# Kernel optimization log

Measured on AMD Instinct MI355X. Metric: run time of the kernel, lower is better.

## Reference

```python
import jax, jax.numpy as jnp
import numpy as np
import math

B, S, HID = 2, 2048, 512
HEADS = 8
DH = HID // HEADS  # 64


def _euler_alpha(seq_len, dh):
    # alpha[t, i] = t * 10000^(-2i/dh), shape [S, dh//2]
    pos = jnp.arange(seq_len, dtype=jnp.float32)[:, None]
    ids = jnp.arange(dh // 2, dtype=jnp.float32)
    freq = jnp.power(10000.0, -2.0 * ids / dh)
    return pos * freq  # [S, dh//2]


def euler_rotate(x, delta):
    # x: [B, H, S, DH] -> polar rotation (EulerFormer, type='ro', no bias b)
    r = x[..., ::2]
    p = x[..., 1::2]
    lam = jnp.sqrt(r * r + p * p)
    theta = jnp.arctan2(p, r) * delta + _euler_alpha(x.shape[2], x.shape[3])[None, None]
    r2 = lam * jnp.cos(theta)
    p2 = lam * jnp.sin(theta)
    # interleave back: stack last dim then reshape
    out = jnp.stack([r2, p2], axis=-1)
    return out.reshape(x.shape)


def setup_inputs() -> dict:
    key = jax.random.key(0)
    ks = jax.random.split(key, 12)
    sc = 1.0 / math.sqrt(HID)
    return {
        "q": jax.random.normal(ks[0], (B, S, HID), jnp.float32),
        "k": jax.random.normal(ks[1], (B, S, HID), jnp.float32),
        "v": jax.random.normal(ks[2], (B, S, HID), jnp.float32),
        "Wq": jax.random.normal(ks[3], (HID, HID), jnp.float32) * sc,
        "bq": jnp.zeros((HID,), jnp.float32),
        "Wk": jax.random.normal(ks[4], (HID, HID), jnp.float32) * sc,
        "bk": jnp.zeros((HID,), jnp.float32),
        "Wv": jax.random.normal(ks[5], (HID, HID), jnp.float32) * sc,
        "bv": jnp.zeros((HID,), jnp.float32),
        "Wo": jax.random.normal(ks[6], (HID, HID), jnp.float32) * sc,
        "bo": jnp.zeros((HID,), jnp.float32),
        "delta_q": jnp.ones((1,), jnp.float32),
        "delta_k": jnp.ones((1,), jnp.float32),
    }


def reference(q, k, v, Wq, bq, Wk, bk, Wv, bv, Wo, bo, delta_q, delta_k):
    b = q.shape[0]
    def proj(x, W, bias):
        y = x @ W.T + bias  # torch Linear: x W^T + b
        return y.reshape(b, -1, HEADS, DH).transpose(0, 2, 1, 3)  # [B,H,S,DH]
    qh = proj(q, Wq, bq)
    kh = proj(k, Wk, bk)
    vh = proj(v, Wv, bv)
    qh = euler_rotate(qh, delta_q)
    kh = euler_rotate(kh, delta_k)
    corr = jnp.einsum('bhqd,bhkd->bhqk', qh, kh) / math.sqrt(DH)
    s = corr.shape[-1]
    causal = jnp.triu(jnp.full((s, s), -jnp.inf, jnp.float32), k=1)
    corr = corr + causal[None, None]
    attn = jax.nn.softmax(corr, axis=-1)
    hidden = jnp.einsum('bhqk,bhkd->bhqd', attn, vh)
    hidden = hidden.transpose(0, 2, 1, 3).reshape(b, -1, HID)
    return hidden @ Wo.T + bo
```

## Files before the change

kernel.cpp:

```cpp
#include <hip/hip_runtime.h>
#include <math.h>

constexpr int B_   = 2;
constexpr int S_   = 2048;
constexpr int HID_ = 512;
constexpr int H_   = 8;
constexpr int DH_  = 64;
constexpr int M_   = B_ * S_;

typedef unsigned short ushort_t;
typedef unsigned int   uint_t;
typedef __attribute__((ext_vector_type(4))) float  f32x4;
typedef __attribute__((ext_vector_type(8))) __bf16 bf16x8;
typedef __attribute__((ext_vector_type(4))) uint_t u32x4;

#define MFMA16(A, Bv, C) __builtin_amdgcn_mfma_f32_16x16x32_bf16( \
    __builtin_bit_cast(bf16x8, (A)), __builtin_bit_cast(bf16x8, (Bv)), (C), 0, 0, 0)

__device__ __forceinline__ uint2 splitPair(float x0, float x1) {
    uint_t b0 = __float_as_uint(x0), b1 = __float_as_uint(x1);
    uint_t hi = (b0 >> 16) | (b1 & 0xFFFF0000u);
    float h0 = __uint_as_float(b0 & 0xFFFF0000u);
    float h1 = __uint_as_float(b1 & 0xFFFF0000u);
    uint_t l0 = __float_as_uint(x0 - h0), l1 = __float_as_uint(x1 - h1);
    uint_t lo = (l0 >> 16) | (l1 & 0xFFFF0000u);
    return make_uint2(hi, lo);
}

template <int MODE>
__device__ __forceinline__ void gemm_mfma_body(const float* __restrict__ A,
                                               const float* __restrict__ W,
                                               const float* __restrict__ bias,
                                               float* __restrict__ out)
{
    constexpr int K_ = HID_;
    __shared__ __align__(16) ushort_t Ah[64][40],  Al[64][40];
    __shared__ __align__(16) ushort_t Bh[128][40], Bl[128][40];

    const int t    = threadIdx.x;
    const int lane = t & 63;
    const int wid  = t >> 6;
    const int wr   = wid >> 1;
    const int wc   = wid & 1;
    const int a    = lane & 15;
    const int g    = lane >> 4;
    const int bm   = blockIdx.x * 64;
    const int bn   = blockIdx.y * 128;

    f32x4 acc[2][4];
#pragma unroll
    for (int mt = 0; mt < 2; ++mt)
#pragma unroll
        for (int nt = 0; nt < 4; ++nt)
#pragma unroll
            for (int r = 0; r < 4; ++r) acc[mt][nt][r] = 0.f;

    const int arow = t >> 2, ag8 = t & 3;

    for (int k0 = 0; k0 < K_; k0 += 32) {
        __syncthreads();
        {
            const float* p = A + (size_t)(bm + arow) * K_ + k0 + ag8 * 8;
            const float4 x0 = *(const float4*)p;
            const float4 x1 = *(const float4*)(p + 4);
            const uint2 s0 = splitPair(x0.x, x0.y), s1 = splitPair(x0.z, x0.w);
            const uint2 s2 = splitPair(x1.x, x1.y), s3 = splitPair(x1.z, x1.w);
            *(u32x4*)&Ah[arow][ag8 * 8] = u32x4{s0.x, s1.x, s2.x, s3.x};
            *(u32x4*)&Al[arow][ag8 * 8] = u32x4{s0.y, s1.y, s2.y, s3.y};
        }
#pragma unroll
        for (int i = 0; i < 2; ++i) {
            const int seg = t + i * 256;
            const int row = seg >> 2, g8 = seg & 3;
            const float* p = W + (size_t)(bn + row) * K_ + k0 + g8 * 8;
            const float4 x0 = *(const float4*)p;
            const float4 x1 = *(const float4*)(p + 4);
            const uint2 s0 = splitPair(x0.x, x0.y), s1 = splitPair(x0.z, x0.w);
            const uint2 s2 = splitPair(x1.x, x1.y), s3 = splitPair(x1.z, x1.w);
            *(u32x4*)&Bh[row][g8 * 8] = u32x4{s0.x, s1.x, s2.x, s3.x};
            *(u32x4*)&Bl[row][g8 * 8] = u32x4{s0.y, s1.y, s2.y, s3.y};
        }
        __syncthreads();

        u32x4 afh[2], afl[2];
#pragma unroll
        for (int mt = 0; mt < 2; ++mt) {
            const int ar = wr * 32 + mt * 16 + a;
            afh[mt] = *(const u32x4*)&Ah[ar][g * 8];
            afl[mt] = *(const u32x4*)&Al[ar][g * 8];
        }
#pragma unroll
        for (int nt = 0; nt < 4; ++nt) {
            const int br = wc * 64 + nt * 16 + a;
            const u32x4 bfh = *(const u32x4*)&Bh[br][g * 8];
            const u32x4 bfl = *(const u32x4*)&Bl[br][g * 8];
#pragma unroll
            for (int mt = 0; mt < 2; ++mt) {
                acc[mt][nt] = MFMA16(afh[mt], bfh, acc[mt][nt]);
                acc[mt][nt] = MFMA16(afh[mt], bfl, acc[mt][nt]);
                acc[mt][nt] = MFMA16(afl[mt], bfh, acc[mt][nt]);
            }
        }
    }

#pragma unroll
    for (int mt = 0; mt < 2; ++mt) {
#pragma unroll
        for (int nt = 0; nt < 4; ++nt) {
            const int n = bn + wc * 64 + nt * 16 + a;
            const float bb = bias[n];
#pragma unroll
            for (int r = 0; r < 4; ++r) {
                const int m = bm + wr * 32 + mt * 16 + g * 4 + r;
                const float val = acc[mt][nt][r] + bb;
                if (MODE == 0) {
                    out[(size_t)m * HID_ + n] = val;
                } else {
                    const int b = m >> 11;
                    const int s = m & (S_ - 1);
                    const int h = n >> 6;
                    const int d = n & (DH_ - 1);
                    if (MODE == 1)
                        out[(((size_t)b * H_ + h) * S_ + s) * DH_ + d] = val;
                    else
                        out[(((size_t)b * H_ + h) * DH_ + d) * S_ + s] = val;
                }
            }
        }
    }
}

struct QkvPtrs {
    const float* A[3];
    const float* W[3];
    const float* bias[3];
    float*       out[3];
};

__global__ __launch_bounds__(256)
void gemm_qkv_kernel(QkvPtrs p)
{
    const int z = blockIdx.z;
    if (z == 2) gemm_mfma_body<2>(p.A[2], p.W[2], p.bias[2], p.out[2]);
    else        gemm_mfma_body<1>(p.A[z], p.W[z], p.bias[z], p.out[z]);
}

__global__ __launch_bounds__(256)
void gemm_out_kernel(const float* __restrict__ A, const float* __restrict__ W,
                     const float* __restrict__ bias, float* __restrict__ out)
{
    gemm_mfma_body<0>(A, W, bias, out);
}

__global__ __launch_bounds__(256)
void euler_rot_kernel(float* __restrict__ qh, float* __restrict__ kh,
                      const float* __restrict__ dq, const float* __restrict__ dk)
{
    constexpr int NP = B_ * H_ * S_ * (DH_ / 2);
    const int idx = blockIdx.x * 256 + threadIdx.x;

    float* x; float delta; int pi;
    if (idx < NP) { x = qh; delta = dq[0]; pi = idx; }
    else          { x = kh; delta = dk[0]; pi = idx - NP; }

    const int i = pi & 31;
    const int s = (pi >> 5) & (S_ - 1);
    const float freq = exp2f(-(float)i * 0.4152410118609203f);

    const float2 rp = ((const float2*)x)[pi];
    const float lam = sqrtf(rp.x * rp.x + rp.y * rp.y);
    const float th  = atan2f(rp.y, rp.x) * delta + (float)s * freq;
    float sn, cs;
    sincosf(th, &sn, &cs);
    ((float2*)x)[pi] = make_float2(lam * cs, lam * sn);
}

__global__ __launch_bounds__(256)
void attn_mfma_kernel(const float* __restrict__ qh, const float* __restrict__ kh,
                      const float* __restrict__ vt, float* __restrict__ hidden)
{
    __shared__ __align__(16) ushort_t Khi[64][72];
    __shared__ __align__(16) ushort_t Klo[64][72];
    __shared__ __align__(16) ushort_t Vhi[64][72];
    __shared__ __align__(16) ushort_t Vlo[64][72];
    __shared__ __align__(16) ushort_t Ph[4][16][72];
    __shared__ __align__(16) ushort_t Pl[4][16][72];

    const int t    = threadIdx.x;
    const int lane = t & 63;
    const int wid  = t >> 6;
    const int a    = lane & 15;
    const int g    = lane >> 4;
    const int qt   = 31 - blockIdx.x;
    const int bh   = blockIdx.y;

    const float* Qrow = qh + ((size_t)bh * S_ + (size_t)qt * 64 + wid * 16 + a) * DH_;
    u32x4 qhi[2], qlo[2];
#pragma unroll
    for (int kit = 0; kit < 2; ++kit) {
        const float* p = Qrow + kit * 32 + g * 8;
        const float4 x0 = *(const float4*)p;
        const float4 x1 = *(const float4*)(p + 4);
        const uint2 p0 = splitPair(x0.x * 0.125f, x0.y * 0.125f);
        const uint2 p1 = splitPair(x0.z * 0.125f, x0.w * 0.125f);
        const uint2 p2 = splitPair(x1.x * 0.125f, x1.y * 0.125f);
        const uint2 p3 = splitPair(x1.z * 0.125f, x1.w * 0.125f);
        qhi[kit] = u32x4{p0.x, p1.x, p2.x, p3.x};
        qlo[kit] = u32x4{p0.y, p1.y, p2.y, p3.y};
    }

    f32x4 Oacc[4];
#pragma unroll
    for (int nt = 0; nt < 4; ++nt)
#pragma unroll
        for (int r = 0; r < 4; ++r) Oacc[nt][r] = 0.f;
    float mrow[4] = {-INFINITY, -INFINITY, -INFINITY, -INFINITY};
    float lrow[4] = {0.f, 0.f, 0.f, 0.f};

    const float4* Kg = (const float4*)(kh + (size_t)bh * S_ * DH_);
    const float*  Vg = vt + (size_t)bh * DH_ * S_;

    for (int kt = 0; kt <= qt; ++kt) {
        __syncthreads();
#pragma unroll
        for (int i = 0; i < 4; ++i) {
            const int flat = t + i * 256;
            const int key = flat >> 4, d4 = (flat & 15) * 4;
            const float4 kv = Kg[kt * 1024 + flat];
            const uint2 s01 = splitPair(kv.x, kv.y);
            const uint2 s23 = splitPair(kv.z, kv.w);
            *(uint2*)&Khi[key][d4] = make_uint2(s01.x, s23.x);
            *(uint2*)&Klo[key][d4] = make_uint2(s01.y, s23.y);
        }
#pragma unroll
        for (int i = 0; i < 4; ++i) {
            const int flat = t + i * 256;
            const int dh = flat >> 4, k4 = (flat & 15) * 4;
            const float4 vv = *(const float4*)(Vg + (size_t)dh * S_ + kt * 64 + k4);
            const uint2 s01 = splitPair(vv.x, vv.y);
            const uint2 s23 = splitPair(vv.z, vv.w);
            *(uint2*)&Vhi[dh][k4] = make_uint2(s01.x, s23.x);
            *(uint2*)&Vlo[dh][k4] = make_uint2(s01.y, s23.y);
        }
        __syncthreads();

        f32x4 Sacc[4];
#pragma unroll
        for (int nt = 0; nt < 4; ++nt)
#pragma unroll
            for (int r = 0; r < 4; ++r) Sacc[nt][r] = 0.f;
#pragma unroll
        for (int kit = 0; kit < 2; ++kit) {
#pragma unroll
            for (int nt = 0; nt < 4; ++nt) {
                const u32x4 kbh = *(const u32x4*)&Khi[a + 16 * nt][kit * 32 + g * 8];
                const u32x4 kbl = *(const u32x4*)&Klo[a + 16 * nt][kit * 32 + g * 8];
                Sacc[nt] = MFMA16(qhi[kit], kbh, Sacc[nt]);
                Sacc[nt] = MFMA16(qhi[kit], kbl, Sacc[nt]);
                Sacc[nt] = MFMA16(qlo[kit], kbh, Sacc[nt]);
            }
        }

        float sc[4][4];
        const int q0 = qt * 64 + wid * 16 + g * 4;
        const int k0 = kt * 64 + a;
#pragma unroll
        for (int nt = 0; nt < 4; ++nt)
#pragma unroll
            for (int r = 0; r < 4; ++r)
                sc[nt][r] = (k0 + 16 * nt <= q0 + r) ? Sacc[nt][r] : -INFINITY;

#pragma unroll
        for (int r = 0; r < 4; ++r) {
            float mr = fmaxf(fmaxf(sc[0][r], sc[1][r]), fmaxf(sc[2][r], sc[3][r]));
            mr = fmaxf(mr, __shfl_xor(mr, 1));
            mr = fmaxf(mr, __shfl_xor(mr, 2));
            mr = fmaxf(mr, __shfl_xor(mr, 4));
            mr = fmaxf(mr, __shfl_xor(mr, 8));
            const float mnew = fmaxf(mrow[r], mr);
            const float fac  = __expf(mrow[r] - mnew);
            mrow[r] = mnew;
            float ps = 0.f;
            const int q = g * 4 + r;
#pragma unroll
            for (int nt = 0; nt < 4; ++nt) {
                const float p = __expf(sc[nt][r] - mnew);
                ps += p;
                const uint_t pb = __float_as_uint(p);
                Ph[wid][q][a + 16 * nt] = (ushort_t)(pb >> 16);
                const float phf = __uint_as_float(pb & 0xFFFF0000u);
                Pl[wid][q][a + 16 * nt] = (ushort_t)(__float_as_uint(p - phf) >> 16);
            }
            lrow[r] = lrow[r] * fac + ps;
#pragma unroll
            for (int nt = 0; nt < 4; ++nt) Oacc[nt][r] *= fac;
        }

#pragma unroll
        for (int kit = 0; kit < 2; ++kit) {
            const u32x4 pah = *(const u32x4*)&Ph[wid][a][kit * 32 + g * 8];
            const u32x4 pal = *(const u32x4*)&Pl[wid][a][kit * 32 + g * 8];
#pragma unroll
            for (int nt = 0; nt < 4; ++nt) {
                const u32x4 vbh = *(const u32x4*)&Vhi[a + 16 * nt][kit * 32 + g * 8];
                const u32x4 vbl = *(const u32x4*)&Vlo[a + 16 * nt][kit * 32 + g * 8];
                Oacc[nt] = MFMA16(pah, vbh, Oacc[nt]);
                Oacc[nt] = MFMA16(pah, vbl, Oacc[nt]);
                Oacc[nt] = MFMA16(pal, vbh, Oacc[nt]);
            }
        }
    }

    float inv[4];
#pragma unroll
    for (int r = 0; r < 4; ++r) {
        float ls = lrow[r];
        ls += __shfl_xor(ls, 1);
        ls += __shfl_xor(ls, 2);
        ls += __shfl_xor(ls, 4);
        ls += __shfl_xor(ls, 8);
        inv[r] = 1.f / ls;
    }
    const int b = bh >> 3, h = bh & 7;
#pragma unroll
    for (int r = 0; r < 4; ++r) {
        const int qg = qt * 64 + wid * 16 + g * 4 + r;
        float* dst = hidden + ((size_t)b * S_ + qg) * HID_ + h * DH_ + a;
#pragma unroll
        for (int nt = 0; nt < 4; ++nt) dst[16 * nt] = Oacc[nt][r] * inv[r];
    }
}

extern "C" void kernel_launch(void* const* d_in, const int* in_sizes, int n_in,
                              void* d_out, int out_size, void* d_ws, size_t ws_size,
                              hipStream_t stream)
{
    const float* q  = (const float*)d_in[0];
    const float* k  = (const float*)d_in[1];
    const float* v  = (const float*)d_in[2];
    const float* Wq = (const float*)d_in[3];
    const float* bq = (const float*)d_in[4];
    const float* Wk = (const float*)d_in[5];
    const float* bk = (const float*)d_in[6];
    const float* Wv = (const float*)d_in[7];
    const float* bv = (const float*)d_in[8];
    const float* Wo = (const float*)d_in[9];
    const float* bo = (const float*)d_in[10];
    const float* dq = (const float*)d_in[11];
    const float* dk = (const float*)d_in[12];
    float* out = (float*)d_out;

    float* ws = (float*)d_ws;
    const size_t TEN = (size_t)B_ * S_ * HID_;
    float* qh     = ws;
    float* kh     = ws + TEN;
    float* vtr    = ws + 2 * TEN;
    float* hidden = ws + 3 * TEN;

    QkvPtrs p;
    p.A[0] = q; p.W[0] = Wq; p.bias[0] = bq; p.out[0] = qh;
    p.A[1] = k; p.W[1] = Wk; p.bias[1] = bk; p.out[1] = kh;
    p.A[2] = v; p.W[2] = Wv; p.bias[2] = bv; p.out[2] = vtr;

    gemm_qkv_kernel<<<dim3(M_ / 64, HID_ / 128, 3), 256, 0, stream>>>(p);
    euler_rot_kernel<<<(2 * B_ * H_ * S_ * (DH_ / 2)) / 256, 256, 0, stream>>>(qh, kh, dq, dk);
    attn_mfma_kernel<<<dim3(S_ / 64, B_ * H_), 256, 0, stream>>>(qh, kh, vtr, hidden);
    gemm_out_kernel<<<dim3(M_ / 64, HID_ / 128), 256, 0, stream>>>(hidden, Wo, bo, out);
}
```

Before: 268.7 us.

## Fuse Euler rotation and bf16 hi/lo split into QKV GEMM epilogue

Moves the Euler polar rotation and the Q scaling into the QKV projection epilogue, pairing values across lanes with a shuffle. The GEMM now writes pre-split bf16 hi/lo tensors, so the separate rotation kernel goes away and attention loads ready-made fragments instead of converting fp32 on every tile. The GEMM tile shrinks from 64x128 to 64x64 to launch more blocks, and the next K-slice is prefetched into registers while the current one is stored to shared memory. Risks: scattered 2-byte stores in the epilogue, and the trig work now runs inside the GEMM blocks.

```diff
diff --git a/kernel.cpp b/kernel.cpp
--- a/kernel.cpp
+++ b/kernel.cpp
@@ -27,15 +27,25 @@
     return make_uint2(hi, lo);
 }
 
+__device__ __forceinline__ void splitOne(float x, ushort_t& hi, ushort_t& lo) {
+    uint_t b = __float_as_uint(x);
+    hi = (ushort_t)(b >> 16);
+    float h = __uint_as_float(b & 0xFFFF0000u);
+    lo = (ushort_t)(__float_as_uint(x - h) >> 16);
+}
+
 template <int MODE>
 __device__ __forceinline__ void gemm_mfma_body(const float* __restrict__ A,
                                                const float* __restrict__ W,
                                                const float* __restrict__ bias,
-                                               float* __restrict__ out)
+                                               ushort_t* __restrict__ outHi,
+                                               ushort_t* __restrict__ outLo,
+                                               float* __restrict__ outF,
+                                               const float* __restrict__ delta)
 {
     constexpr int K_ = HID_;
-    __shared__ __align__(16) ushort_t Ah[64][40],  Al[64][40];
-    __shared__ __align__(16) ushort_t Bh[128][40], Bl[128][40];
+    __shared__ __align__(16) ushort_t Ah[64][40], Al[64][40];
+    __shared__ __align__(16) ushort_t Bh[64][40], Bl[64][40];
 
     const int t    = threadIdx.x;
     const int lane = t & 63;
@@ -45,44 +55,44 @@
     const int a    = lane & 15;
     const int g    = lane >> 4;
     const int bm   = blockIdx.x * 64;
-    const int bn   = blockIdx.y * 128;
-
-    f32x4 acc[2][4];
+    const int bn   = blockIdx.y * 64;
+
+    const int srow = t >> 2, sg8 = t & 3;
+    const float* Ap = A + (size_t)(bm + srow) * K_ + sg8 * 8;
+    const float* Wp = W + (size_t)(bn + srow) * K_ + sg8 * 8;
+
+    float4 ra0 = *(const float4*)Ap,       ra1 = *(const float4*)(Ap + 4);
+    float4 rb0 = *(const float4*)Wp,       rb1 = *(const float4*)(Wp + 4);
+
+    f32x4 acc[2][2];
 #pragma unroll
     for (int mt = 0; mt < 2; ++mt)
 #pragma unroll
-        for (int nt = 0; nt < 4; ++nt)
+        for (int nt = 0; nt < 2; ++nt)
 #pragma unroll
             for (int r = 0; r < 4; ++r) acc[mt][nt][r] = 0.f;
-
-    const int arow = t >> 2, ag8 = t & 3;
 
     for (int k0 = 0; k0 < K_; k0 += 32) {
         __syncthreads();
         {
-            const float* p = A + (size_t)(bm + arow) * K_ + k0 + ag8 * 8;
-            const float4 x0 = *(const float4*)p;
-            const float4 x1 = *(const float4*)(p + 4);
-            const uint2 s0 = splitPair(x0.x, x0.y), s1 = splitPair(x0.z, x0.w);
-            const uint2 s2 = splitPair(x1.x, x1.y), s3 = splitPair(x1.z, x1.w);
-            *(u32x4*)&Ah[arow][ag8 * 8] = u32x4{s0.x, s1.x, s2.x, s3.x};
-            *(u32x4*)&Al[arow][ag8 * 8] = u32x4{s0.y, s1.y, s2.y, s3.y};
-        }
-#pragma unroll
-        for (int i = 0; i < 2; ++i) {
-            const int seg = t + i * 256;
-            const int row = seg >> 2, g8 = seg & 3;
-            const float* p = W + (size_t)(bn + row) * K_ + k0 + g8 * 8;
-            const float4 x0 = *(const float4*)p;
-            const float4 x1 = *(const float4*)(p + 4);
-            const uint2 s0 = splitPair(x0.x, x0.y), s1 = splitPair(x0.z, x0.w);
-            const uint2 s2 = splitPair(x1.x, x1.y), s3 = splitPair(x1.z, x1.w);
-            *(u32x4*)&Bh[row][g8 * 8] = u32x4{s0.x, s1.x, s2.x, s3.x};
-            *(u32x4*)&Bl[row][g8 * 8] = u32x4{s0.y, s1.y, s2.y, s3.y};
+            const uint2 s0 = splitPair(ra0.x, ra0.y), s1 = splitPair(ra0.z, ra0.w);
+            const uint2 s2 = splitPair(ra1.x, ra1.y), s3 = splitPair(ra1.z, ra1.w);
+            *(u32x4*)&Ah[srow][sg8 * 8] = u32x4{s0.x, s1.x, s2.x, s3.x};
+            *(u32x4*)&Al[srow][sg8 * 8] = u32x4{s0.y, s1.y, s2.y, s3.y};
+            const uint2 t0 = splitPair(rb0.x, rb0.y), t1 = splitPair(rb0.z, rb0.w);
+            const uint2 t2 = splitPair(rb1.x, rb1.y), t3 = splitPair(rb1.z, rb1.w);
+            *(u32x4*)&Bh[srow][sg8 * 8] = u32x4{t0.x, t1.x, t2.x, t3.x};
+            *(u32x4*)&Bl[srow][sg8 * 8] = u32x4{t0.y, t1.y, t2.y, t3.y};
+        }
+        if (k0 + 32 < K_) {
+            const float* pa = Ap + k0 + 32;
+            const float* pw = Wp + k0 + 32;
+            ra0 = *(const float4*)pa; ra1 = *(const float4*)(pa + 4);
+            rb0 = *(const float4*)pw; rb1 = *(const float4*)(pw + 4);
         }
         __syncthreads();
 
-        u32x4 afh[2], afl[2];
+        u32x4 afh[2], afl[2], bfh[2], bfl[2];
 #pragma unroll
         for (int mt = 0; mt < 2; ++mt) {
             const int ar = wr * 32 + mt * 16 + a;
@@ -90,41 +100,72 @@
             afl[mt] = *(const u32x4*)&Al[ar][g * 8];
         }
 #pragma unroll
-        for (int nt = 0; nt < 4; ++nt) {
-            const int br = wc * 64 + nt * 16 + a;
-            const u32x4 bfh = *(const u32x4*)&Bh[br][g * 8];
-            const u32x4 bfl = *(const u32x4*)&Bl[br][g * 8];
+        for (int nt = 0; nt < 2; ++nt) {
+            const int br = wc * 32 + nt * 16 + a;
+            bfh[nt] = *(const u32x4*)&Bh[br][g * 8];
+            bfl[nt] = *(const u32x4*)&Bl[br][g * 8];
+        }
+#pragma unroll
+        for (int nt = 0; nt < 2; ++nt)
 #pragma unroll
             for (int mt = 0; mt < 2; ++mt) {
-                acc[mt][nt] = MFMA16(afh[mt], bfh, acc[mt][nt]);
-                acc[mt][nt] = MFMA16(afh[mt], bfl, acc[mt][nt]);
-                acc[mt][nt] = MFMA16(afl[mt], bfh, acc[mt][nt]);
-            }
-        }
-    }
-
+                acc[mt][nt] = MFMA16(afh[mt], bfh[nt], acc[mt][nt]);
+                acc[mt][nt] = MFMA16(afh[mt], bfl[nt], acc[mt][nt]);
+                acc[mt][nt] = MFMA16(afl[mt], bfh[nt], acc[mt][nt]);
+            }
+    }
+
+    const float del = (MODE == 1 || MODE == 2) ? delta[0] : 0.f;
 #pragma unroll
     for (int mt = 0; mt < 2; ++mt) {
 #pragma unroll
-        for (int nt = 0; nt < 4; ++nt) {
-            const int n = bn + wc * 64 + nt * 16 + a;
+        for (int nt = 0; nt < 2; ++nt) {
+            const int n  = bn + wc * 32 + nt * 16 + a;
             const float bb = bias[n];
-#pragma unroll
-            for (int r = 0; r < 4; ++r) {
-                const int m = bm + wr * 32 + mt * 16 + g * 4 + r;
-                const float val = acc[mt][nt][r] + bb;
-                if (MODE == 0) {
-                    out[(size_t)m * HID_ + n] = val;
-                } else {
-                    const int b = m >> 11;
-                    const int s = m & (S_ - 1);
-                    const int h = n >> 6;
-                    const int d = n & (DH_ - 1);
-                    if (MODE == 1)
-                        out[(((size_t)b * H_ + h) * S_ + s) * DH_ + d] = val;
-                    else
-                        out[(((size_t)b * H_ + h) * DH_ + d) * S_ + s] = val;
+            f32x4 vals;
+#pragma unroll
+            for (int r = 0; r < 4; ++r) vals[r] = acc[mt][nt][r] + bb;
+
+            if (MODE == 0) {
+#pragma unroll
+                for (int r = 0; r < 4; ++r) {
+                    const int m = bm + wr * 32 + mt * 16 + g * 4 + r;
+                    outF[(size_t)m * HID_ + n] = vals[r];
                 }
+            } else if (MODE == 1 || MODE == 2) {
+                const int d  = n & 63;
+                const int h  = n >> 6;
+                const float freq = exp2f(-(float)(d >> 1) * 0.4152410118609203f);
+#pragma unroll
+                for (int r = 0; r < 4; ++r) {
+                    const int m = bm + wr * 32 + mt * 16 + g * 4 + r;
+                    const int b = m >> 11, s = m & (S_ - 1);
+                    const float val  = vals[r];
+                    const float part = __shfl_xor(val, 1);
+                    const float rr = (a & 1) ? part : val;
+                    const float pp = (a & 1) ? val  : part;
+                    const float lam = sqrtf(rr * rr + pp * pp);
+                    const float th  = atan2f(pp, rr) * del + (float)s * freq;
+                    float sn, cs;
+                    sincosf(th, &sn, &cs);
+                    float o = (a & 1) ? lam * sn : lam * cs;
+                    if (MODE == 1) o *= 0.125f;
+                    ushort_t hi, lo;
+                    splitOne(o, hi, lo);
+                    const size_t idx = (((size_t)b * H_ + h) * S_ + s) * DH_ + d;
+                    outHi[idx] = hi;
+                    outLo[idx] = lo;
+                }
+            } else {
+                const int d  = n & 63;
+                const int h  = n >> 6;
+                const int m0 = bm + wr * 32 + mt * 16 + g * 4;
+                const int b  = m0 >> 11, s0 = m0 & (S_ - 1);
+                const uint2 p01 = splitPair(vals[0], vals[1]);
+                const uint2 p23 = splitPair(vals[2], vals[3]);
+                const size_t idx = (((size_t)b * H_ + h) * DH_ + d) * S_ + s0;
+                *(uint2*)&outHi[idx] = make_uint2(p01.x, p23.x);
+                *(uint2*)&outLo[idx] = make_uint2(p01.y, p23.y);
             }
         }
     }
@@ -134,50 +175,32 @@
     const float* A[3];
     const float* W[3];
     const float* bias[3];
-    float*       out[3];
+    ushort_t*    hi[3];
+    ushort_t*    lo[3];
+    const float* del[2];
 };
 
 __global__ __launch_bounds__(256)
 void gemm_qkv_kernel(QkvPtrs p)
 {
     const int z = blockIdx.z;
-    if (z == 2) gemm_mfma_body<2>(p.A[2], p.W[2], p.bias[2], p.out[2]);
-    else        gemm_mfma_body<1>(p.A[z], p.W[z], p.bias[z], p.out[z]);
+    if (z == 0)      gemm_mfma_body<1>(p.A[0], p.W[0], p.bias[0], p.hi[0], p.lo[0], nullptr, p.del[0]);
+    else if (z == 1) gemm_mfma_body<2>(p.A[1], p.W[1], p.bias[1], p.hi[1], p.lo[1], nullptr, p.del[1]);
+    else             gemm_mfma_body<3>(p.A[2], p.W[2], p.bias[2], p.hi[2], p.lo[2], nullptr, nullptr);
 }
 
 __global__ __launch_bounds__(256)
 void gemm_out_kernel(const float* __restrict__ A, const float* __restrict__ W,
                      const float* __restrict__ bias, float* __restrict__ out)
 {
-    gemm_mfma_body<0>(A, W, bias, out);
+    gemm_mfma_body<0>(A, W, bias, nullptr, nullptr, out, nullptr);
 }
 
 __global__ __launch_bounds__(256)
-void euler_rot_kernel(float* __restrict__ qh, float* __restrict__ kh,
-                      const float* __restrict__ dq, const float* __restrict__ dk)
-{
-    constexpr int NP = B_ * H_ * S_ * (DH_ / 2);
-    const int idx = blockIdx.x * 256 + threadIdx.x;
-
-    float* x; float delta; int pi;
-    if (idx < NP) { x = qh; delta = dq[0]; pi = idx; }
-    else          { x = kh; delta = dk[0]; pi = idx - NP; }
-
-    const int i = pi & 31;
-    const int s = (pi >> 5) & (S_ - 1);
-    const float freq = exp2f(-(float)i * 0.4152410118609203f);
-
-    const float2 rp = ((const float2*)x)[pi];
-    const float lam = sqrtf(rp.x * rp.x + rp.y * rp.y);
-    const float th  = atan2f(rp.y, rp.x) * delta + (float)s * freq;
-    float sn, cs;
-    sincosf(th, &sn, &cs);
-    ((float2*)x)[pi] = make_float2(lam * cs, lam * sn);
-}
-
-__global__ __launch_bounds__(256)
-void attn_mfma_kernel(const float* __restrict__ qh, const float* __restrict__ kh,
-                      const float* __restrict__ vt, float* __restrict__ hidden)
+void attn_mfma_kernel(const ushort_t* __restrict__ qhi_g, const ushort_t* __restrict__ qlo_g,
+                      const ushort_t* __restrict__ khi_g, const ushort_t* __restrict__ klo_g,
+                      const ushort_t* __restrict__ vhi_g, const ushort_t* __restrict__ vlo_g,
+                      float* __restrict__ hidden)
 {
     __shared__ __align__(16) ushort_t Khi[64][72];
     __shared__ __align__(16) ushort_t Klo[64][72];
@@ -194,19 +217,14 @@
     const int qt   = 31 - blockIdx.x;
     const int bh   = blockIdx.y;
 
-    const float* Qrow = qh + ((size_t)bh * S_ + (size_t)qt * 64 + wid * 16 + a) * DH_;
     u32x4 qhi[2], qlo[2];
-#pragma unroll
-    for (int kit = 0; kit < 2; ++kit) {
-        const float* p = Qrow + kit * 32 + g * 8;
-        const float4 x0 = *(const float4*)p;
-        const float4 x1 = *(const float4*)(p + 4);
-        const uint2 p0 = splitPair(x0.x * 0.125f, x0.y * 0.125f);
-        const uint2 p1 = splitPair(x0.z * 0.125f, x0.w * 0.125f);
-        const uint2 p2 = splitPair(x1.x * 0.125f, x1.y * 0.125f);
-        const uint2 p3 = splitPair(x1.z * 0.125f, x1.w * 0.125f);
-        qhi[kit] = u32x4{p0.x, p1.x, p2.x, p3.x};
-        qlo[kit] = u32x4{p0.y, p1.y, p2.y, p3.y};
+    {
+        const size_t qrow = ((size_t)bh * S_ + (size_t)qt * 64 + wid * 16 + a) * DH_;
+#pragma unroll
+        for (int kit = 0; kit < 2; ++kit) {
+            qhi[kit] = *(const u32x4*)&qhi_g[qrow + kit * 32 + g * 8];
+            qlo[kit] = *(const u32x4*)&qlo_g[qrow + kit * 32 + g * 8];
+        }
     }
 
     f32x4 Oacc[4];
@@ -217,30 +235,20 @@
     float mrow[4] = {-INFINITY, -INFINITY, -INFINITY, -INFINITY};
     float lrow[4] = {0.f, 0.f, 0.f, 0.f};
 
-    const float4* Kg = (const float4*)(kh + (size_t)bh * S_ * DH_);
-    const float*  Vg = vt + (size_t)bh * DH_ * S_;
-
     for (int kt = 0; kt <= qt; ++kt) {
+        const ushort_t* Ksh = khi_g + ((size_t)bh * S_ + kt * 64) * DH_;
+        const ushort_t* Ksl = klo_g + ((size_t)bh * S_ + kt * 64) * DH_;
+        const ushort_t* Vsh = vhi_g + (size_t)bh * DH_ * S_ + kt * 64;
+        const ushort_t* Vsl = vlo_g + (size_t)bh * DH_ * S_ + kt * 64;
         __syncthreads();
 #pragma unroll
-        for (int i = 0; i < 4; ++i) {
-            const int flat = t + i * 256;
-            const int key = flat >> 4, d4 = (flat & 15) * 4;
-            const float4 kv = Kg[kt * 1024 + flat];
-            const uint2 s01 = splitPair(kv.x, kv.y);
-            const uint2 s23 = splitPair(kv.z, kv.w);
-            *(uint2*)&Khi[key][d4] = make_uint2(s01.x, s23.x);
-            *(uint2*)&Klo[key][d4] = make_uint2(s01.y, s23.y);
-        }
-#pragma unroll
-        for (int i = 0; i < 4; ++i) {
-            const int flat = t + i * 256;
-            const int dh = flat >> 4, k4 = (flat & 15) * 4;
-            const float4 vv = *(const float4*)(Vg + (size_t)dh * S_ + kt * 64 + k4);
-            const uint2 s01 = splitPair(vv.x, vv.y);
-            const uint2 s23 = splitPair(vv.z, vv.w);
-            *(uint2*)&Vhi[dh][k4] = make_uint2(s01.x, s23.x);
-            *(uint2*)&Vlo[dh][k4] = make_uint2(s01.y, s23.y);
+        for (int i = 0; i < 2; ++i) {
+            const int seg = t + i * 256;
+            const int row = seg >> 3, c8 = (seg & 7) * 8;
+            *(u32x4*)&Khi[row][c8] = *(const u32x4*)&Ksh[row * 64 + c8];
+            *(u32x4*)&Klo[row][c8] = *(const u32x4*)&Ksl[row * 64 + c8];
+            *(u32x4*)&Vhi[row][c8] = *(const u32x4*)&Vsh[(size_t)row * S_ + c8];
+            *(u32x4*)&Vlo[row][c8] = *(const u32x4*)&Vsl[(size_t)row * S_ + c8];
         }
         __syncthreads();
 
@@ -286,10 +294,10 @@
             for (int nt = 0; nt < 4; ++nt) {
                 const float p = __expf(sc[nt][r] - mnew);
                 ps += p;
-                const uint_t pb = __float_as_uint(p);
-                Ph[wid][q][a + 16 * nt] = (ushort_t)(pb >> 16);
-                const float phf = __uint_as_float(pb & 0xFFFF0000u);
-                Pl[wid][q][a + 16 * nt] = (ushort_t)(__float_as_uint(p - phf) >> 16);
+                ushort_t phi, plo;
+                splitOne(p, phi, plo);
+                Ph[wid][q][a + 16 * nt] = phi;
+                Pl[wid][q][a + 16 * nt] = plo;
             }
             lrow[r] = lrow[r] * fac + ps;
 #pragma unroll
@@ -350,20 +358,22 @@
     const float* dk = (const float*)d_in[12];
     float* out = (float*)d_out;
 
-    float* ws = (float*)d_ws;
     const size_t TEN = (size_t)B_ * S_ * HID_;
-    float* qh     = ws;
-    float* kh     = ws + TEN;
-    float* vtr    = ws + 2 * TEN;
-    float* hidden = ws + 3 * TEN;
+    ushort_t* qhi = (ushort_t*)d_ws;
+    ushort_t* qlo = qhi + TEN;
+    ushort_t* khi = qlo + TEN;
+    ushort_t* klo = khi + TEN;
+    ushort_t* vhi = klo + TEN;
+    ushort_t* vlo = vhi + TEN;
+    float* hidden = (float*)(vlo + TEN);
 
     QkvPtrs p;
-    p.A[0] = q; p.W[0] = Wq; p.bias[0] = bq; p.out[0] = qh;
-    p.A[1] = k; p.W[1] = Wk; p.bias[1] = bk; p.out[1] = kh;
-    p.A[2] = v; p.W[2] = Wv; p.bias[2] = bv; p.out[2] = vtr;
-
-    gemm_qkv_kernel<<<dim3(M_ / 64, HID_ / 128, 3), 256, 0, stream>>>(p);
-    euler_rot_kernel<<<(2 * B_ * H_ * S_ * (DH_ / 2)) / 256, 256, 0, stream>>>(qh, kh, dq, dk);
-    attn_mfma_kernel<<<dim3(S_ / 64, B_ * H_), 256, 0, stream>>>(qh, kh, vtr, hidden);
-    gemm_out_kernel<<<dim3(M_ / 64, HID_ / 128), 256, 0, stream>>>(hidden, Wo, bo, out);
-}
+    p.A[0] = q; p.W[0] = Wq; p.bias[0] = bq; p.hi[0] = qhi; p.lo[0] = qlo;
+    p.A[1] = k; p.W[1] = Wk; p.bias[1] = bk; p.hi[1] = khi; p.lo[1] = klo;
+    p.A[2] = v; p.W[2] = Wv; p.bias[2] = bv; p.hi[2] = vhi; p.lo[2] = vlo;
+    p.del[0] = dq; p.del[1] = dk;
+
+    gemm_qkv_kernel<<<dim3(M_ / 64, HID_ / 64, 3), 256, 0, stream>>>(p);
+    attn_mfma_kernel<<<dim3(S_ / 64, B_ * H_), 256, 0, stream>>>(qhi, qlo, khi, klo, vhi, vlo, hidden);
+    gemm_out_kernel<<<dim3(M_ / 64, HID_ / 64), 256, 0, stream>>>(hidden, Wo, bo, out);
+}
```

Result: faster. 243.0 us (-9.5%).
